# Kernel optimization log

Hardware: AMD Instinct MI355X
Metric: run time of the kernel (lower is better)

The kernel has to match this reference:

```python
import jax, jax.numpy as jnp
import numpy as np

T, B, D = 2048, 256, 32
H0, H1, O = 64, 64, 35


def _fastgrnn_scan(xs, h0, W, U, bg, bu, zeta, nu):
    """Run FastGRNN recurrence. xs: [T, N, Din], h0: [N, H] -> hiddenStates [T, N, H].
    z = sigmoid(xW + hU + bg); c = tanh(xW + hU + bu);
    h = z*h + (sigmoid(zeta)*(1-z) + sigmoid(nu))*c
    """
    zs = jax.nn.sigmoid(zeta)  # [1,1]
    ns = jax.nn.sigmoid(nu)    # [1,1]
    xW = jnp.einsum('tnd,dh->tnh', xs, W)  # precompute input projections (same math)

    def step(h, xw):
        pre = xw + h @ U
        z = jax.nn.sigmoid(pre + bg)
        c = jnp.tanh(pre + bu)
        h_new = z * h + (zs * (1.0 - z) + ns) * c
        return h_new, h_new

    _, hs = jax.lax.scan(step, h0, xW)
    return hs


def setup_inputs() -> dict:
    key = jax.random.key(0)
    ks = jax.random.split(key, 8)
    x = jax.random.normal(ks[0], (T, B, D), dtype=jnp.float32)
    # FastGRNNCell params, layer 0 (inputDim -> hiddenDim0), full-rank (wRank=uRank=None)
    W0 = 0.1 * jax.random.normal(ks[1], (D, H0), dtype=jnp.float32)
    U0 = 0.1 * jax.random.normal(ks[2], (H0, H0), dtype=jnp.float32)
    bg0 = jnp.ones((1, H0), jnp.float32)
    bu0 = jnp.ones((1, H0), jnp.float32)
    zeta0 = 1.0 * jnp.ones((1, 1), jnp.float32)
    nu0 = -4.0 * jnp.ones((1, 1), jnp.float32)
    # layer 1 (hiddenDim0 -> hiddenDim1)
    W1 = 0.1 * jax.random.normal(ks[3], (H0, H1), dtype=jnp.float32)
    U1 = 0.1 * jax.random.normal(ks[4], (H1, H1), dtype=jnp.float32)
    bg1 = jnp.ones((1, H1), jnp.float32)
    bu1 = jnp.ones((1, H1), jnp.float32)
    zeta1 = 1.0 * jnp.ones((1, 1), jnp.float32)
    nu1 = -4.0 * jnp.ones((1, 1), jnp.float32)
    # output projection
    Wout = jax.random.normal(ks[5], (H1, O), dtype=jnp.float32)
    Bout = jax.random.normal(ks[6], (O,), dtype=jnp.float32)
    return {
        'x': x, 'brickSize': 32,
        'W0': W0, 'U0': U0, 'bg0': bg0, 'bu0': bu0, 'zeta0': zeta0, 'nu0': nu0,
        'W1': W1, 'U1': U1, 'bg1': bg1, 'bu1': bu1, 'zeta1': zeta1, 'nu1': nu1,
        'Wout': Wout, 'Bout': Bout,
    }


def reference(x, brickSize, W0, U0, bg0, bu0, zeta0, nu0,
              W1, U1, bg1, bu1, zeta1, nu1, Wout, Bout):
    t, b, d = x.shape
    numBricks = t // brickSize
    x = x[:numBricks * brickSize]
    # brick: [numBricks, brickSize, B, D] -> [brickSize, numBricks*B, D]
    xb = x.reshape(numBricks, brickSize, b, d)
    xb = jnp.transpose(xb, (1, 0, 2, 3)).reshape(brickSize, numBricks * b, d)
    # layer-0 FastGRNN over the brick time axis
    h0_init = jnp.zeros((numBricks * b, W0.shape[1]), x.dtype)
    hs0 = _fastgrnn_scan(xb, h0_init, W0, U0, bg0, bu0, zeta0, nu0)
    last0 = hs0[-1].reshape(numBricks, b, W0.shape[1])  # [numBricks, B, H0]
    # layer-1 FastGRNN over the brick axis
    h1_init = jnp.zeros((b, W1.shape[1]), x.dtype)
    hs1 = _fastgrnn_scan(last0, h1_init, W1, U1, bg1, bu1, zeta1, nu1)
    out = hs1[-1] @ Wout + Bout  # [B, outputDim]
    return out
```

## Files before the change

### kernel.cpp

```cpp
#include <hip/hip_runtime.h>
#include <hip/hip_bf16.h>


#define NB    64
#define BS    32
#define BATCH 256
#define D0    32
#define H     64
#define OUTD  35
#define LOG2E 1.44269504088896340736f

typedef _Float16 h4    __attribute__((ext_vector_type(4)));
typedef __fp16   hf2   __attribute__((ext_vector_type(2)));
typedef float    f32x4 __attribute__((ext_vector_type(4)));

union HB { h4 v; hf2 h[2]; unsigned u[2]; };

__device__ __forceinline__ float rcp_fast(float x) {
    return __builtin_amdgcn_rcpf(x);
}
__device__ __forceinline__ float sigm(float x) {
    return rcp_fast(1.0f + __expf(-x));
}
__device__ __forceinline__ void lds_barrier() {
    asm volatile("s_waitcnt lgkmcnt(0)\n\ts_barrier" ::: "memory");
}

__device__ __forceinline__ void act_update(float pre, float bgp, float Ku,
                                           float zs, float zns, float& hcr) {
    float t  = fminf(fmaxf(pre, -12.f), 12.f);
    float a  = exp2f(fmaf(t, -LOG2E, bgp));
    float b  = a * a * Ku;
    float da = 1.f + a, db = 1.f + b;
    float rr = rcp_fast(da * db);
    float z  = rr * db;
    float ib = rr * da;
    float c  = fmaf(2.f, ib, -1.f);
    float w  = fmaf(-zs, z, zns);
    hcr = fmaf(z, hcr, w * c);
}

__global__ __launch_bounds__(64, 2) void l0_kernel(
    const float* __restrict__ x,
    const float* __restrict__ W,
    const float* __restrict__ U,
    const float* __restrict__ bg,
    const float* __restrict__ bu,
    const float* __restrict__ zeta,
    const float* __restrict__ nu,
    unsigned* __restrict__ last0pk)
{
    const int lane = threadIdx.x;
    const int l15  = lane & 15;
    const int lg   = lane >> 4;

    const int brick     = blockIdx.x >> 4;
    const int batchbase = (blockIdx.x & 15) << 4;

    h4 Wt[4][2], Ut[4][4];
#pragma unroll
    for (int T = 0; T < 4; ++T) {
        const int u = 16 * T + l15;
#pragma unroll
        for (int c = 0; c < 2; ++c)
#pragma unroll
            for (int j = 0; j < 4; ++j)
                Wt[T][c][j] = (_Float16)W[(16 * c + 4 * lg + j) * H + u];
#pragma unroll
        for (int c = 0; c < 4; ++c)
#pragma unroll
            for (int j = 0; j < 4; ++j)
                Ut[T][c][j] = (_Float16)U[(16 * c + 4 * lg + j) * H + u];
    }

    float bgp[4][4], Ku[4][4];
#pragma unroll
    for (int T = 0; T < 4; ++T)
#pragma unroll
        for (int r = 0; r < 4; ++r) {
            int u = 16 * T + 4 * lg + r;
            float g = bg[u], q = bu[u];
            bgp[T][r] = -LOG2E * g;
            Ku[T][r]  = exp2f(2.f * LOG2E * (g - q));
        }

    const float zs  = sigm(zeta[0]);
    const float ns  = sigm(nu[0]);
    const float zns = zs + ns;

    float hc[4][4];
#pragma unroll
    for (int T = 0; T < 4; ++T)
#pragma unroll
        for (int r = 0; r < 4; ++r) hc[T][r] = 0.f;

    HB hbf[4];
#pragma unroll
    for (int c = 0; c < 4; ++c) { hbf[c].u[0] = 0; hbf[c].u[1] = 0; }

    const float* xb = x + ((size_t)(brick * BS) * BATCH + batchbase + l15) * D0 + 4 * lg;
    const size_t xstep = (size_t)BATCH * D0;

    float4 c0 = reinterpret_cast<const float4*>(xb)[0];
    float4 c1 = reinterpret_cast<const float4*>(xb + 16)[0];
    float4 n0 = reinterpret_cast<const float4*>(xb + xstep)[0];
    float4 n1 = reinterpret_cast<const float4*>(xb + xstep + 16)[0];

#pragma unroll 1
    for (int t = 0; t < BS; ++t) {
        const int tp = (t + 2 < BS) ? (t + 2) : (BS - 1);
        float4 p0 = reinterpret_cast<const float4*>(xb + (size_t)tp * xstep)[0];
        float4 p1 = reinterpret_cast<const float4*>(xb + (size_t)tp * xstep + 16)[0];

        HB xf0, xf1;
        xf0.h[0] = __builtin_amdgcn_cvt_pkrtz(c0.x, c0.y);
        xf0.h[1] = __builtin_amdgcn_cvt_pkrtz(c0.z, c0.w);
        xf1.h[0] = __builtin_amdgcn_cvt_pkrtz(c1.x, c1.y);
        xf1.h[1] = __builtin_amdgcn_cvt_pkrtz(c1.z, c1.w);

        f32x4 acc[4];
#pragma unroll
        for (int T = 0; T < 4; ++T) {
            f32x4 a = {0.f, 0.f, 0.f, 0.f};
            a = __builtin_amdgcn_mfma_f32_16x16x16f16(Wt[T][0], xf0.v, a, 0, 0, 0);
            a = __builtin_amdgcn_mfma_f32_16x16x16f16(Wt[T][1], xf1.v, a, 0, 0, 0);
#pragma unroll
            for (int c = 0; c < 4; ++c)
                a = __builtin_amdgcn_mfma_f32_16x16x16f16(Ut[T][c], hbf[c].v, a, 0, 0, 0);
            acc[T] = a;
        }

#pragma unroll
        for (int T = 0; T < 4; ++T)
#pragma unroll
            for (int r = 0; r < 4; ++r)
                act_update(acc[T][r], bgp[T][r], Ku[T][r], zs, zns, hc[T][r]);

#pragma unroll
        for (int c = 0; c < 4; ++c) {
            hbf[c].h[0] = __builtin_amdgcn_cvt_pkrtz(hc[c][0], hc[c][1]);
            hbf[c].h[1] = __builtin_amdgcn_cvt_pkrtz(hc[c][2], hc[c][3]);
        }

        c0 = n0; c1 = n1;
        n0 = p0; n1 = p1;
    }

#pragma unroll
    for (int T = 0; T < 4; ++T) {
        size_t idx = ((((size_t)brick * 4 + T) * 4 + lg) * 256 + batchbase + l15) * 2;
        *reinterpret_cast<uint2*>(&last0pk[idx]) = make_uint2(hbf[T].u[0], hbf[T].u[1]);
    }
}

__global__ __launch_bounds__(256, 2) void l1_kernel(
    const unsigned* __restrict__ last0pk,
    const float* __restrict__ W,
    const float* __restrict__ U,
    const float* __restrict__ bg,
    const float* __restrict__ bu,
    const float* __restrict__ zeta,
    const float* __restrict__ nu,
    const float* __restrict__ Wout,
    const float* __restrict__ Bout,
    float* __restrict__ out)
{
    __shared__ unsigned hx[2][4][4][16][2];
    __shared__ float hsf[16][H];

    const int tid  = threadIdx.x;
    const int lane = tid & 63;
    const int T    = __builtin_amdgcn_readfirstlane(tid >> 6);
    const int l15  = lane & 15;
    const int lg   = lane >> 4;

    const int batchbase = blockIdx.x << 4;

    for (int i = tid; i < 1024; i += 256) (&hx[0][0][0][0][0])[i] = 0;

    h4 Wt[4], Ut[4];
#pragma unroll
    for (int c = 0; c < 4; ++c) {
        const int u = 16 * T + l15;
#pragma unroll
        for (int j = 0; j < 4; ++j) {
            Wt[c][j] = (_Float16)W[(16 * c + 4 * lg + j) * H + u];
            Ut[c][j] = (_Float16)U[(16 * c + 4 * lg + j) * H + u];
        }
    }
    float bgp[4], Ku[4];
#pragma unroll
    for (int r = 0; r < 4; ++r) {
        int u = 16 * T + 4 * lg + r;
        float g = bg[u], q = bu[u];
        bgp[r] = -LOG2E * g;
        Ku[r]  = exp2f(2.f * LOG2E * (g - q));
    }

    const float zs  = sigm(zeta[0]);
    const float ns  = sigm(nu[0]);
    const float zns = zs + ns;

    float hc[4] = {0.f, 0.f, 0.f, 0.f};

#define XIDX(t, c) (((((size_t)(t) * 4 + (c)) * 4 + lg) * 256 + batchbase + l15) * 2)
    uint2 xc[4], xn[4], xp[4];
#pragma unroll
    for (int c = 0; c < 4; ++c) {
        xc[c] = *reinterpret_cast<const uint2*>(&last0pk[XIDX(0, c)]);
        xn[c] = *reinterpret_cast<const uint2*>(&last0pk[XIDX(1, c)]);
    }

    __syncthreads();

    int buf = 0;
#pragma unroll 1
    for (int t = 0; t < NB; ++t) {
        const int tp = (t + 2 < NB) ? (t + 2) : (NB - 1);
#pragma unroll
        for (int c = 0; c < 4; ++c)
            xp[c] = *reinterpret_cast<const uint2*>(&last0pk[XIDX(tp, c)]);

        HB hf[4];
#pragma unroll
        for (int c = 0; c < 4; ++c) {
            uint2 v = *reinterpret_cast<const uint2*>(&hx[buf][c][lg][l15][0]);
            hf[c].u[0] = v.x; hf[c].u[1] = v.y;
        }

        f32x4 ax = {0.f, 0.f, 0.f, 0.f};
        f32x4 ah = {0.f, 0.f, 0.f, 0.f};
#pragma unroll
        for (int c = 0; c < 4; ++c) {
            HB xv; xv.u[0] = xc[c].x; xv.u[1] = xc[c].y;
            ax = __builtin_amdgcn_mfma_f32_16x16x16f16(Wt[c], xv.v, ax, 0, 0, 0);
        }
#pragma unroll
        for (int c = 0; c < 4; ++c)
            ah = __builtin_amdgcn_mfma_f32_16x16x16f16(Ut[c], hf[c].v, ah, 0, 0, 0);

        HB ho;
#pragma unroll
        for (int r = 0; r < 4; ++r)
            act_update(ax[r] + ah[r], bgp[r], Ku[r], zs, zns, hc[r]);
        ho.h[0] = __builtin_amdgcn_cvt_pkrtz(hc[0], hc[1]);
        ho.h[1] = __builtin_amdgcn_cvt_pkrtz(hc[2], hc[3]);

        *reinterpret_cast<uint2*>(&hx[buf ^ 1][T][lg][l15][0]) = make_uint2(ho.u[0], ho.u[1]);
        lds_barrier();
        buf ^= 1;
#pragma unroll
        for (int c = 0; c < 4; ++c) { xc[c] = xn[c]; xn[c] = xp[c]; }
    }
#undef XIDX

#pragma unroll
    for (int r = 0; r < 4; ++r) hsf[l15][16 * T + 4 * lg + r] = hc[r];
    __syncthreads();

    for (int p = tid; p < 16 * OUTD; p += 256) {
        int s = p / OUTD;
        int o = p - s * OUTD;
        float a = Bout[o];
#pragma unroll
        for (int u = 0; u < H; ++u) a = fmaf(hsf[s][u], Wout[u * OUTD + o], a);
        out[(size_t)(batchbase + s) * OUTD + o] = a;
    }
}

extern "C" void kernel_launch(void* const* d_in, const int* in_sizes, int n_in,
                              void* d_out, int out_size, void* d_ws, size_t ws_size,
                              hipStream_t stream) {
    const float* x    = (const float*)d_in[0];
    const float* W0   = (const float*)d_in[2];
    const float* U0   = (const float*)d_in[3];
    const float* bg0  = (const float*)d_in[4];
    const float* bu0  = (const float*)d_in[5];
    const float* z0   = (const float*)d_in[6];
    const float* n0   = (const float*)d_in[7];
    const float* W1   = (const float*)d_in[8];
    const float* U1   = (const float*)d_in[9];
    const float* bg1  = (const float*)d_in[10];
    const float* bu1  = (const float*)d_in[11];
    const float* z1   = (const float*)d_in[12];
    const float* n1   = (const float*)d_in[13];
    const float* Wout = (const float*)d_in[14];
    const float* Bout = (const float*)d_in[15];
    float* out = (float*)d_out;

    unsigned* last0pk = (unsigned*)d_ws;

    l0_kernel<<<1024, 64, 0, stream>>>(x, W0, U0, bg0, bu0, z0, n0, last0pk);
    l1_kernel<<<16, 256, 0, stream>>>(last0pk, W1, U1, bg1, bu1, z1, n1, Wout, Bout, out);
}
```

Baseline: 82.37 us.

## Split layer-0 recurrence across two waves with bf16 MFMA and swizzled LDS hidden state

Layer 0 now uses two wavefronts per block, each owning 32 hidden units. They exchange the bf16 hidden state through a double-buffered, XOR-swizzled LDS tile with a barrier every step, and use 16x16x32 bf16 MFMAs instead of 16x16x16 f16. The activation switches to separate sigmoid and tanh without clamping. The intermediate layout becomes row-major f16, and layer 1 packs two batch groups per 512-thread block. The aim is to shorten the serial per-step chain by halving each wave's MFMA and activation work, at the cost of a barrier per step and bf16 precision loss in the recurrence.

```diff
diff --git a/kernel.cpp b/kernel.cpp
--- a/kernel.cpp
+++ b/kernel.cpp
@@ -10,11 +10,13 @@
 #define OUTD  35
 #define LOG2E 1.44269504088896340736f
 
+typedef short    bf8   __attribute__((ext_vector_type(8)));
 typedef _Float16 h4    __attribute__((ext_vector_type(4)));
 typedef __fp16   hf2   __attribute__((ext_vector_type(2)));
 typedef float    f32x4 __attribute__((ext_vector_type(4)));
 
 union HB { h4 v; hf2 h[2]; unsigned u[2]; };
+union U4BF8 { unsigned u[4]; bf8 v; };
 
 __device__ __forceinline__ float rcp_fast(float x) {
     return __builtin_amdgcn_rcpf(x);
@@ -22,10 +24,32 @@
 __device__ __forceinline__ float sigm(float x) {
     return rcp_fast(1.0f + __expf(-x));
 }
+__device__ __forceinline__ float tanh_fast(float x) {
+    float q = rcp_fast(1.0f + __expf(-2.0f * x));
+    return fmaf(2.0f, q, -1.0f);
+}
+__device__ __forceinline__ short f2bf(float f) {
+    __hip_bfloat16 b = __float2bfloat16(f);
+    return __builtin_bit_cast(short, b);
+}
+__device__ __forceinline__ unsigned pk2bf(float lo, float hi) {
+    __hip_bfloat162 h2 = __float22bfloat162_rn(make_float2(lo, hi));
+    unsigned r;
+    __builtin_memcpy(&r, &h2, 4);
+    return r;
+}
+__device__ __forceinline__ unsigned pk2f16(float lo, float hi) {
+    hf2 h2 = __builtin_amdgcn_cvt_pkrtz(lo, hi);
+    unsigned r;
+    __builtin_memcpy(&r, &h2, 4);
+    return r;
+}
 __device__ __forceinline__ void lds_barrier() {
     asm volatile("s_waitcnt lgkmcnt(0)\n\ts_barrier" ::: "memory");
 }
-
+__device__ __forceinline__ int swz_x(int s) {
+    return ((s & 7) << 4) ^ ((s & 8) << 2);
+}
 __device__ __forceinline__ void act_update(float pre, float bgp, float Ku,
                                            float zs, float zns, float& hcr) {
     float t  = fminf(fmaxf(pre, -12.f), 12.f);
@@ -40,7 +64,7 @@
     hcr = fmaf(z, hcr, w * c);
 }
 
-__global__ __launch_bounds__(64, 2) void l0_kernel(
+__global__ __launch_bounds__(128, 2) void l0_kernel(
     const float* __restrict__ x,
     const float* __restrict__ W,
     const float* __restrict__ U,
@@ -48,113 +72,126 @@
     const float* __restrict__ bu,
     const float* __restrict__ zeta,
     const float* __restrict__ nu,
-    unsigned* __restrict__ last0pk)
+    unsigned short* __restrict__ last0)
 {
-    const int lane = threadIdx.x;
+    __shared__ unsigned char hb[2][16 * 128];
+
+    const int tid  = threadIdx.x;
+    const int lane = tid & 63;
+    const int w    = __builtin_amdgcn_readfirstlane(tid >> 6);
     const int l15  = lane & 15;
     const int lg   = lane >> 4;
 
     const int brick     = blockIdx.x >> 4;
     const int batchbase = (blockIdx.x & 15) << 4;
 
-    h4 Wt[4][2], Ut[4][4];
-#pragma unroll
-    for (int T = 0; T < 4; ++T) {
-        const int u = 16 * T + l15;
-#pragma unroll
-        for (int c = 0; c < 2; ++c)
-#pragma unroll
-            for (int j = 0; j < 4; ++j)
-                Wt[T][c][j] = (_Float16)W[(16 * c + 4 * lg + j) * H + u];
-#pragma unroll
-        for (int c = 0; c < 4; ++c)
-#pragma unroll
-            for (int j = 0; j < 4; ++j)
-                Ut[T][c][j] = (_Float16)U[(16 * c + 4 * lg + j) * H + u];
-    }
-
-    float bgp[4][4], Ku[4][4];
-#pragma unroll
-    for (int T = 0; T < 4; ++T)
-#pragma unroll
-        for (int r = 0; r < 4; ++r) {
-            int u = 16 * T + 4 * lg + r;
-            float g = bg[u], q = bu[u];
-            bgp[T][r] = -LOG2E * g;
-            Ku[T][r]  = exp2f(2.f * LOG2E * (g - q));
-        }
+    *reinterpret_cast<float4*>(&hb[0][tid * 16]) = make_float4(0.f, 0.f, 0.f, 0.f);
+
+    bf8 Wb[2], Ub0[2], Ub1[2];
+    float bgc[2], buc[2];
+#pragma unroll
+    for (int T = 0; T < 2; ++T) {
+        const int uc = 32 * w + 16 * T + l15;
+#pragma unroll
+        for (int j = 0; j < 8; ++j) {
+            Wb[T][j]  = f2bf(W[(8 * lg + j) * H + uc]);
+            Ub0[T][j] = f2bf(U[(8 * lg + j) * H + uc]);
+            Ub1[T][j] = f2bf(U[(32 + 8 * lg + j) * H + uc]);
+        }
+        bgc[T] = bg[uc];
+        buc[T] = bu[uc];
+    }
 
     const float zs  = sigm(zeta[0]);
     const float ns  = sigm(nu[0]);
     const float zns = zs + ns;
 
-    float hc[4][4];
-#pragma unroll
-    for (int T = 0; T < 4; ++T)
+    float hc[2][4];
+#pragma unroll
+    for (int T = 0; T < 2; ++T)
 #pragma unroll
         for (int r = 0; r < 4; ++r) hc[T][r] = 0.f;
 
-    HB hbf[4];
-#pragma unroll
-    for (int c = 0; c < 4; ++c) { hbf[c].u[0] = 0; hbf[c].u[1] = 0; }
-
-    const float* xb = x + ((size_t)(brick * BS) * BATCH + batchbase + l15) * D0 + 4 * lg;
+    const float* xbase = x + ((size_t)(brick * BS) * BATCH + batchbase + l15) * D0 + 8 * lg;
     const size_t xstep = (size_t)BATCH * D0;
 
-    float4 c0 = reinterpret_cast<const float4*>(xb)[0];
-    float4 c1 = reinterpret_cast<const float4*>(xb + 16)[0];
-    float4 n0 = reinterpret_cast<const float4*>(xb + xstep)[0];
-    float4 n1 = reinterpret_cast<const float4*>(xb + xstep + 16)[0];
-
+    float4 xa0 = reinterpret_cast<const float4*>(xbase)[0];
+    float4 xa1 = reinterpret_cast<const float4*>(xbase)[1];
+    float4 xn0 = reinterpret_cast<const float4*>(xbase + xstep)[0];
+    float4 xn1 = reinterpret_cast<const float4*>(xbase + xstep)[1];
+
+    int woff[2][4];
+#pragma unroll
+    for (int T = 0; T < 2; ++T)
+#pragma unroll
+        for (int r = 0; r < 4; ++r) {
+            int s = 4 * lg + r;
+            woff[T][r] = s * 128 + (((32 * w + 16 * T + l15) * 2) ^ swz_x(s));
+        }
+    const int rswz = swz_x(l15);
+
+    __syncthreads();
+
+    int cur = 0;
 #pragma unroll 1
     for (int t = 0; t < BS; ++t) {
         const int tp = (t + 2 < BS) ? (t + 2) : (BS - 1);
-        float4 p0 = reinterpret_cast<const float4*>(xb + (size_t)tp * xstep)[0];
-        float4 p1 = reinterpret_cast<const float4*>(xb + (size_t)tp * xstep + 16)[0];
-
-        HB xf0, xf1;
-        xf0.h[0] = __builtin_amdgcn_cvt_pkrtz(c0.x, c0.y);
-        xf0.h[1] = __builtin_amdgcn_cvt_pkrtz(c0.z, c0.w);
-        xf1.h[0] = __builtin_amdgcn_cvt_pkrtz(c1.x, c1.y);
-        xf1.h[1] = __builtin_amdgcn_cvt_pkrtz(c1.z, c1.w);
-
-        f32x4 acc[4];
-#pragma unroll
-        for (int T = 0; T < 4; ++T) {
+        float4 p0 = reinterpret_cast<const float4*>(xbase + (size_t)tp * xstep)[0];
+        float4 p1 = reinterpret_cast<const float4*>(xbase + (size_t)tp * xstep)[1];
+
+        U4BF8 xp;
+        xp.u[0] = pk2bf(xa0.x, xa0.y);
+        xp.u[1] = pk2bf(xa0.z, xa0.w);
+        xp.u[2] = pk2bf(xa1.x, xa1.y);
+        xp.u[3] = pk2bf(xa1.z, xa1.w);
+
+        const unsigned char* hr = &hb[cur][l15 * 128];
+        bf8 ha0 = *reinterpret_cast<const bf8*>(hr + ((16 * lg) ^ rswz));
+        bf8 ha1 = *reinterpret_cast<const bf8*>(hr + ((64 + 16 * lg) ^ rswz));
+
+        unsigned char* wb = &hb[cur ^ 1][0];
+#pragma unroll
+        for (int T = 0; T < 2; ++T) {
             f32x4 a = {0.f, 0.f, 0.f, 0.f};
-            a = __builtin_amdgcn_mfma_f32_16x16x16f16(Wt[T][0], xf0.v, a, 0, 0, 0);
-            a = __builtin_amdgcn_mfma_f32_16x16x16f16(Wt[T][1], xf1.v, a, 0, 0, 0);
-#pragma unroll
-            for (int c = 0; c < 4; ++c)
-                a = __builtin_amdgcn_mfma_f32_16x16x16f16(Ut[T][c], hbf[c].v, a, 0, 0, 0);
-            acc[T] = a;
-        }
-
-#pragma unroll
-        for (int T = 0; T < 4; ++T)
-#pragma unroll
-            for (int r = 0; r < 4; ++r)
-                act_update(acc[T][r], bgp[T][r], Ku[T][r], zs, zns, hc[T][r]);
-
-#pragma unroll
-        for (int c = 0; c < 4; ++c) {
-            hbf[c].h[0] = __builtin_amdgcn_cvt_pkrtz(hc[c][0], hc[c][1]);
-            hbf[c].h[1] = __builtin_amdgcn_cvt_pkrtz(hc[c][2], hc[c][3]);
-        }
-
-        c0 = n0; c1 = n1;
-        n0 = p0; n1 = p1;
-    }
-
-#pragma unroll
-    for (int T = 0; T < 4; ++T) {
-        size_t idx = ((((size_t)brick * 4 + T) * 4 + lg) * 256 + batchbase + l15) * 2;
-        *reinterpret_cast<uint2*>(&last0pk[idx]) = make_uint2(hbf[T].u[0], hbf[T].u[1]);
-    }
-}
-
-__global__ __launch_bounds__(256, 2) void l1_kernel(
-    const unsigned* __restrict__ last0pk,
+            a = __builtin_amdgcn_mfma_f32_16x16x32_bf16(xp.v, Wb[T], a, 0, 0, 0);
+            a = __builtin_amdgcn_mfma_f32_16x16x32_bf16(ha0, Ub0[T], a, 0, 0, 0);
+            a = __builtin_amdgcn_mfma_f32_16x16x32_bf16(ha1, Ub1[T], a, 0, 0, 0);
+
+#pragma unroll
+            for (int r = 0; r < 4; ++r) {
+                float z = sigm(a[r] + bgc[T]);
+                float c = tanh_fast(a[r] + buc[T]);
+                float wq = fmaf(-zs, z, zns);
+                hc[T][r] = fmaf(z, hc[T][r], wq * c);
+            }
+            unsigned pkA = pk2bf(hc[T][0], hc[T][1]);
+            unsigned pkB = pk2bf(hc[T][2], hc[T][3]);
+            *reinterpret_cast<unsigned short*>(wb + woff[T][0]) = (unsigned short)pkA;
+            *reinterpret_cast<unsigned short*>(wb + woff[T][1]) = (unsigned short)(pkA >> 16);
+            *reinterpret_cast<unsigned short*>(wb + woff[T][2]) = (unsigned short)pkB;
+            *reinterpret_cast<unsigned short*>(wb + woff[T][3]) = (unsigned short)(pkB >> 16);
+        }
+        lds_barrier();
+        cur ^= 1;
+        xa0 = xn0; xa1 = xn1;
+        xn0 = p0;  xn1 = p1;
+    }
+
+#pragma unroll
+    for (int T = 0; T < 2; ++T) {
+        unsigned pkA = pk2f16(hc[T][0], hc[T][1]);
+        unsigned pkB = pk2f16(hc[T][2], hc[T][3]);
+        const int uc = 32 * w + 16 * T + l15;
+        unsigned short* op = last0 + ((size_t)(brick * BATCH + batchbase)) * H + uc;
+        op[(size_t)(4 * lg + 0) * H] = (unsigned short)pkA;
+        op[(size_t)(4 * lg + 1) * H] = (unsigned short)(pkA >> 16);
+        op[(size_t)(4 * lg + 2) * H] = (unsigned short)pkB;
+        op[(size_t)(4 * lg + 3) * H] = (unsigned short)(pkB >> 16);
+    }
+}
+
+__global__ __launch_bounds__(512, 2) void l1_kernel(
+    const unsigned short* __restrict__ last0,
     const float* __restrict__ W,
     const float* __restrict__ U,
     const float* __restrict__ bg,
@@ -165,18 +202,19 @@
     const float* __restrict__ Bout,
     float* __restrict__ out)
 {
-    __shared__ unsigned hx[2][4][4][16][2];
-    __shared__ float hsf[16][H];
+    __shared__ unsigned hx[2][2][4][4][16][2];
+    __shared__ float hsf[2][16][H];
 
     const int tid  = threadIdx.x;
     const int lane = tid & 63;
-    const int T    = __builtin_amdgcn_readfirstlane(tid >> 6);
+    const int pair = __builtin_amdgcn_readfirstlane(tid >> 8);
+    const int T    = __builtin_amdgcn_readfirstlane((tid >> 6) & 3);
     const int l15  = lane & 15;
     const int lg   = lane >> 4;
 
-    const int batchbase = blockIdx.x << 4;
-
-    for (int i = tid; i < 1024; i += 256) (&hx[0][0][0][0][0])[i] = 0;
+    const int batchbase = (blockIdx.x << 5) + (pair << 4);
+
+    for (int i = tid; i < 2048; i += 512) (&hx[0][0][0][0][0][0])[i] = 0;
 
     h4 Wt[4], Ut[4];
 #pragma unroll
@@ -203,12 +241,12 @@
 
     float hc[4] = {0.f, 0.f, 0.f, 0.f};
 
-#define XIDX(t, c) (((((size_t)(t) * 4 + (c)) * 4 + lg) * 256 + batchbase + l15) * 2)
+#define XADDR(t, c) (&last0[((size_t)(t) * BATCH + batchbase + l15) * H + 16 * (c) + 4 * lg])
     uint2 xc[4], xn[4], xp[4];
 #pragma unroll
     for (int c = 0; c < 4; ++c) {
-        xc[c] = *reinterpret_cast<const uint2*>(&last0pk[XIDX(0, c)]);
-        xn[c] = *reinterpret_cast<const uint2*>(&last0pk[XIDX(1, c)]);
+        xc[c] = *reinterpret_cast<const uint2*>(XADDR(0, c));
+        xn[c] = *reinterpret_cast<const uint2*>(XADDR(1, c));
     }
 
     __syncthreads();
@@ -219,12 +257,12 @@
         const int tp = (t + 2 < NB) ? (t + 2) : (NB - 1);
 #pragma unroll
         for (int c = 0; c < 4; ++c)
-            xp[c] = *reinterpret_cast<const uint2*>(&last0pk[XIDX(tp, c)]);
+            xp[c] = *reinterpret_cast<const uint2*>(XADDR(tp, c));
 
         HB hf[4];
 #pragma unroll
         for (int c = 0; c < 4; ++c) {
-            uint2 v = *reinterpret_cast<const uint2*>(&hx[buf][c][lg][l15][0]);
+            uint2 v = *reinterpret_cast<const uint2*>(&hx[buf][pair][c][lg][l15][0]);
             hf[c].u[0] = v.x; hf[c].u[1] = v.y;
         }
 
@@ -246,25 +284,27 @@
         ho.h[0] = __builtin_amdgcn_cvt_pkrtz(hc[0], hc[1]);
         ho.h[1] = __builtin_amdgcn_cvt_pkrtz(hc[2], hc[3]);
 
-        *reinterpret_cast<uint2*>(&hx[buf ^ 1][T][lg][l15][0]) = make_uint2(ho.u[0], ho.u[1]);
+        *reinterpret_cast<uint2*>(&hx[buf ^ 1][pair][T][lg][l15][0]) = make_uint2(ho.u[0], ho.u[1]);
         lds_barrier();
         buf ^= 1;
 #pragma unroll
         for (int c = 0; c < 4; ++c) { xc[c] = xn[c]; xn[c] = xp[c]; }
     }
-#undef XIDX
-
-#pragma unroll
-    for (int r = 0; r < 4; ++r) hsf[l15][16 * T + 4 * lg + r] = hc[r];
+#undef XADDR
+
+#pragma unroll
+    for (int r = 0; r < 4; ++r) hsf[pair][l15][16 * T + 4 * lg + r] = hc[r];
     __syncthreads();
 
-    for (int p = tid; p < 16 * OUTD; p += 256) {
-        int s = p / OUTD;
-        int o = p - s * OUTD;
+    for (int p = tid; p < 2 * 16 * OUTD; p += 512) {
+        int pr = p / (16 * OUTD);
+        int q  = p - pr * (16 * OUTD);
+        int s  = q / OUTD;
+        int o  = q - s * OUTD;
         float a = Bout[o];
 #pragma unroll
-        for (int u = 0; u < H; ++u) a = fmaf(hsf[s][u], Wout[u * OUTD + o], a);
-        out[(size_t)(batchbase + s) * OUTD + o] = a;
+        for (int u = 0; u < H; ++u) a = fmaf(hsf[pr][s][u], Wout[u * OUTD + o], a);
+        out[(size_t)((blockIdx.x << 5) + (pr << 4) + s) * OUTD + o] = a;
     }
 }
 
@@ -288,8 +328,8 @@
     const float* Bout = (const float*)d_in[15];
     float* out = (float*)d_out;
 
-    unsigned* last0pk = (unsigned*)d_ws;
-
-    l0_kernel<<<1024, 64, 0, stream>>>(x, W0, U0, bg0, bu0, z0, n0, last0pk);
-    l1_kernel<<<16, 256, 0, stream>>>(last0pk, W1, U1, bg1, bu1, z1, n1, Wout, Bout, out);
-}
+    unsigned short* last0 = (unsigned short*)d_ws;
+
+    l0_kernel<<<1024, 128, 0, stream>>>(x, W0, U0, bg0, bu0, z0, n0, last0);
+    l1_kernel<<<8, 512, 0, stream>>>(last0, W1, U1, bg1, bu1, z1, n1, Wout, Bout, out);
+}
```

Result: slower. 99.72 us (+21.1%).
